# Optimization experiments

Hardware: AMD Instinct MI355X
Metric: run time of the kernel (lower is better)

Reference implementation:

```python
import jax, jax.numpy as jnp
import numpy as np

N_NODES = 50000
N_EDGES = 800000
ENT_DIM = 128
REL_DIM = 128
NUM_REL = 200  # relation table has 2*NUM_REL rows (forward + inverse)


def setup_inputs() -> dict:
    key = jax.random.key(0)
    ks = jax.random.split(key, 16)
    inp = {
        'src': jax.random.randint(ks[0], (N_EDGES,), 0, N_NODES),
        'dst': jax.random.randint(ks[1], (N_EDGES,), 0, N_NODES),
        'etypes': jax.random.randint(ks[2], (N_EDGES,), 0, 2 * NUM_REL),
        'ent_emb': jax.random.normal(ks[3], (N_NODES, ENT_DIM), jnp.float32),
        'rel_emb': jax.random.normal(ks[4], (2 * NUM_REL, REL_DIM), jnp.float32),
        'W_O_w': jax.random.normal(ks[5], (ENT_DIM, REL_DIM + ENT_DIM), jnp.float32) * 0.05,
        'W_O_b': jax.random.normal(ks[6], (ENT_DIM,), jnp.float32) * 0.05,
        'W_I_w': jax.random.normal(ks[7], (ENT_DIM, REL_DIM + ENT_DIM), jnp.float32) * 0.05,
        'W_I_b': jax.random.normal(ks[8], (ENT_DIM,), jnp.float32) * 0.05,
        'W_S_w': jax.random.normal(ks[9], (ENT_DIM, ENT_DIM), jnp.float32) * 0.05,
        'W_S_b': jax.random.normal(ks[10], (ENT_DIM,), jnp.float32) * 0.05,
        'W_R_w': jax.random.normal(ks[11], (REL_DIM, REL_DIM), jnp.float32) * 0.05,
        'W_R_b': jax.random.normal(ks[12], (REL_DIM,), jnp.float32) * 0.05,
    }
    return inp


def reference(src, dst, etypes, ent_emb, rel_emb,
              W_O_w, W_O_b, W_I_w, W_I_b, W_S_w, W_S_b, W_R_w, W_R_b):
    # msg_func: per-edge gather of relation emb and source node emb, concat,
    # then route through W_O (type < num_rel) or W_I (type >= num_rel).
    comp_h = jnp.concatenate([rel_emb[etypes], ent_emb[src]], axis=-1)  # [E, rel+ent]
    msg_o = comp_h @ W_O_w.T + W_O_b  # [E, ent]
    msg_i = comp_h @ W_I_w.T + W_I_b
    non_inv = (etypes < NUM_REL)[:, None]
    msg = jnp.where(non_inv, msg_o, msg_i)
    # fn.mean('msg','h_agg'): scatter-mean into destination nodes (0 if no in-edges)
    agg_sum = jax.ops.segment_sum(msg, dst, num_segments=N_NODES)
    deg = jax.ops.segment_sum(jnp.ones((msg.shape[0],), msg.dtype), dst,
                              num_segments=N_NODES)
    h_agg = agg_sum / jnp.maximum(deg, 1.0)[:, None]
    # apply_node_func (act is None -> identity)
    ent_new = ent_emb @ W_S_w.T + W_S_b + h_agg
    # edge_update
    rel_new = rel_emb @ W_R_w.T + W_R_b
    return ent_new, rel_new
```

## Files before the change

kernel.cpp:

```cpp
#include <hip/hip_runtime.h>
#include <hip/hip_bf16.h>

#define N_NODES 50000
#define N_EDGES 800000
#define DIM 128
#define NUM_REL 200
#define NREL2 (2 * NUM_REL)
#define NROWG (N_NODES / 16)
#define NBLK_G ((NROWG + 3) / 4)
#define FILL_NB 2048
#define NCHUNK_E (N_EDGES / 256)
#define NODES_PER_XCD (N_NODES / 8)
#define CAP 64
#define ZROW (2 * N_NODES)
#define ZREL NREL2
#define ZPAY (ZROW | (ZREL << 17))

typedef __bf16 bf16x8 __attribute__((ext_vector_type(8)));
typedef float f32x4 __attribute__((ext_vector_type(4)));

__global__ void __launch_bounds__(256)
prep_rel_kernel(const float* __restrict__ rel_emb,
                const float* __restrict__ W_O_w, const float* __restrict__ W_O_b,
                const float* __restrict__ W_I_w, const float* __restrict__ W_I_b,
                const float* __restrict__ W_R_w, const float* __restrict__ W_R_b,
                const float* __restrict__ W_S_w,
                __bf16* __restrict__ WTh, __bf16* __restrict__ WTl,
                int* __restrict__ counts, __bf16* __restrict__ EEb,
                __bf16* __restrict__ Rb, float* __restrict__ rel_new) {
    const int bid = blockIdx.x;
    if (bid < NREL2 / 2) {
        __shared__ float row[2][DIM];
        const int h = threadIdx.x >> 7;
        const int j = threadIdx.x & 127;
        const int t = bid * 2 + h;
        row[h][j] = rel_emb[t * DIM + j];
        __syncthreads();

        const bool fwd = (t < NUM_REL);
        const float* __restrict__ wSel = (fwd ? W_O_w : W_I_w) + j * (2 * DIM);
        const float* __restrict__ wR = W_R_w + j * DIM;
        float aSel = 0.f, aR = 0.f;
#pragma unroll 8
        for (int k = 0; k < DIM; ++k) {
            const float e = row[h][k];
            aSel += e * wSel[k];
            aR += e * wR[k];
        }
        Rb[t * DIM + j] = (__bf16)(aSel + (fwd ? W_O_b[j] : W_I_b[j]));
        rel_new[t * DIM + j] = aR + W_R_b[j];
    } else {
        const int idx = (bid - NREL2 / 2) * 256 + threadIdx.x;
        if (idx < 384 * DIM) {
            const int j = idx >> 7;
            const int k = idx & 127;
            float v;
            if (j < 128) v = W_O_w[j * (2 * DIM) + DIM + k];
            else if (j < 256) v = W_I_w[(j - 128) * (2 * DIM) + DIM + k];
            else v = W_S_w[(j - 256) * DIM + k];
            const __bf16 h = (__bf16)v;
            WTh[idx] = h;
            WTl[idx] = (__bf16)(v - (float)h);
        }
        if (idx < N_NODES) counts[idx] = 0;
        if (idx < DIM) {
            EEb[(size_t)ZROW * DIM + idx] = (__bf16)0.f;
            Rb[(size_t)ZREL * DIM + idx] = (__bf16)0.f;
        }
    }
}

#define REP4(F) F(0) F(1) F(2) F(3)

__global__ void __launch_bounds__(256, 1)
gemm_fill_kernel(const float* __restrict__ ent,
                 const __bf16* __restrict__ WTh, const __bf16* __restrict__ WTl,
                 const float* __restrict__ W_S_b,
                 __bf16* __restrict__ EEb, float* __restrict__ ent_S,
                 const int* __restrict__ src, const int* __restrict__ dst,
                 const int* __restrict__ et, int* __restrict__ counts,
                 int* __restrict__ sp) {
    __shared__ __bf16 LBh[16 * 64 * 8];
    __shared__ __bf16 LBl[16 * 64 * 8];

    if (blockIdx.x >= NBLK_G) {
        const int fb = blockIdx.x - NBLK_G;
        const int r = blockIdx.x & 7;
#pragma unroll 1
        for (int c = fb >> 3; c < NCHUNK_E; c += FILL_NB / 8) {
            const int e = c * 256 + threadIdx.x;
            const int d = dst[e];
            if ((unsigned)(d - r * NODES_PER_XCD) < (unsigned)NODES_PER_XCD) {
                const int t = et[e];
                const int row = src[e] + ((t < NUM_REL) ? 0 : N_NODES);
                const int pos = atomicAdd(&counts[d], 1);
                if (pos < CAP) sp[(d << 6) + pos] = row | (t << 17);
            }
        }
        return;
    }

    const int tid = threadIdx.x;
    const int wv = tid >> 6;
    const int rg = blockIdx.x * 4 + wv;
    const bool valid = (rg < NROWG);
    const int rgc = valid ? rg : (NROWG - 1);
    const int l = tid & 63;
    const int r16 = l & 15;
    const int kg = l >> 4;

    const float* __restrict__ aptr = ent + (size_t)(rgc * 16 + r16) * DIM + kg * 8;
#define ADECL(ks)                                                              \
    bf16x8 ah##ks, al##ks;                                                     \
    {                                                                          \
        const float4 v0 = *(const float4*)(aptr + (ks) * 32);                  \
        const float4 v1 = *(const float4*)(aptr + (ks) * 32 + 4);              \
        const float xs[8] = {v0.x, v0.y, v0.z, v0.w, v1.x, v1.y, v1.z, v1.w};  \
        _Pragma("unroll") for (int i = 0; i < 8; ++i) {                        \
            const __bf16 h = (__bf16)xs[i];                                    \
            ah##ks[i] = h;                                                     \
            al##ks[i] = (__bf16)(xs[i] - (float)h);                            \
        }                                                                      \
    }
    REP4(ADECL)
#undef ADECL

    const int orow = rgc * 16 + kg * 4;

#pragma unroll 1
    for (int cb = 0; cb < 6; ++cb) {
        __syncthreads();
#pragma unroll
        for (int i = 0; i < 4; ++i) {
            const int sks = i * 4 + wv;
            const int s = sks >> 2;
            const int ks = sks & 3;
            const size_t soff =
                (size_t)(cb * 64 + s * 16 + r16) * DIM + ks * 32 + kg * 8;
            const int g = i * 256 + tid;
            *(bf16x8*)(&LBh[g * 8]) = *(const bf16x8*)(WTh + soff);
            *(bf16x8*)(&LBl[g * 8]) = *(const bf16x8*)(WTl + soff);
        }
        __syncthreads();

        f32x4 p0 = {0.f, 0.f, 0.f, 0.f}, q0 = {0.f, 0.f, 0.f, 0.f};
        f32x4 p1 = {0.f, 0.f, 0.f, 0.f}, q1 = {0.f, 0.f, 0.f, 0.f};
        f32x4 p2 = {0.f, 0.f, 0.f, 0.f}, q2 = {0.f, 0.f, 0.f, 0.f};
        f32x4 p3 = {0.f, 0.f, 0.f, 0.f}, q3 = {0.f, 0.f, 0.f, 0.f};

#define KS(ks)                                                                 \
    {                                                                          \
        const bf16x8 bh0 = *(const bf16x8*)(&LBh[((0 * 4 + (ks)) * 64 + l) * 8]); \
        const bf16x8 bh1 = *(const bf16x8*)(&LBh[((1 * 4 + (ks)) * 64 + l) * 8]); \
        const bf16x8 bh2 = *(const bf16x8*)(&LBh[((2 * 4 + (ks)) * 64 + l) * 8]); \
        const bf16x8 bh3 = *(const bf16x8*)(&LBh[((3 * 4 + (ks)) * 64 + l) * 8]); \
        const bf16x8 bl0 = *(const bf16x8*)(&LBl[((0 * 4 + (ks)) * 64 + l) * 8]); \
        const bf16x8 bl1 = *(const bf16x8*)(&LBl[((1 * 4 + (ks)) * 64 + l) * 8]); \
        const bf16x8 bl2 = *(const bf16x8*)(&LBl[((2 * 4 + (ks)) * 64 + l) * 8]); \
        const bf16x8 bl3 = *(const bf16x8*)(&LBl[((3 * 4 + (ks)) * 64 + l) * 8]); \
        p0 = __builtin_amdgcn_mfma_f32_16x16x32_bf16(ah##ks, bh0, p0, 0, 0, 0); \
        p1 = __builtin_amdgcn_mfma_f32_16x16x32_bf16(ah##ks, bh1, p1, 0, 0, 0); \
        p2 = __builtin_amdgcn_mfma_f32_16x16x32_bf16(ah##ks, bh2, p2, 0, 0, 0); \
        p3 = __builtin_amdgcn_mfma_f32_16x16x32_bf16(ah##ks, bh3, p3, 0, 0, 0); \
        q0 = __builtin_amdgcn_mfma_f32_16x16x32_bf16(al##ks, bh0, q0, 0, 0, 0); \
        q1 = __builtin_amdgcn_mfma_f32_16x16x32_bf16(al##ks, bh1, q1, 0, 0, 0); \
        q2 = __builtin_amdgcn_mfma_f32_16x16x32_bf16(al##ks, bh2, q2, 0, 0, 0); \
        q3 = __builtin_amdgcn_mfma_f32_16x16x32_bf16(al##ks, bh3, q3, 0, 0, 0); \
        q0 = __builtin_amdgcn_mfma_f32_16x16x32_bf16(ah##ks, bl0, q0, 0, 0, 0); \
        q1 = __builtin_amdgcn_mfma_f32_16x16x32_bf16(ah##ks, bl1, q1, 0, 0, 0); \
        q2 = __builtin_amdgcn_mfma_f32_16x16x32_bf16(ah##ks, bl2, q2, 0, 0, 0); \
        q3 = __builtin_amdgcn_mfma_f32_16x16x32_bf16(ah##ks, bl3, q3, 0, 0, 0); \
    }
        REP4(KS)
#undef KS

        if (valid) {
            const int colb = (cb & 1) * 64;
            if (cb < 4) {
                __bf16* __restrict__ obb =
                    EEb + ((cb < 2) ? 0 : (size_t)N_NODES * DIM);
#define ST(s, P, Q)                                                            \
                {                                                              \
                    const int col = colb + (s) * 16 + r16;                     \
                    const f32x4 a = P + Q;                                     \
                    obb[(size_t)(orow + 0) * DIM + col] = (__bf16)a[0];        \
                    obb[(size_t)(orow + 1) * DIM + col] = (__bf16)a[1];        \
                    obb[(size_t)(orow + 2) * DIM + col] = (__bf16)a[2];        \
                    obb[(size_t)(orow + 3) * DIM + col] = (__bf16)a[3];        \
                }
                ST(0, p0, q0) ST(1, p1, q1) ST(2, p2, q2) ST(3, p3, q3)
#undef ST
            } else {
#define ST(s, P, Q)                                                            \
                {                                                              \
                    const int col = colb + (s) * 16 + r16;                     \
                    const float bs = W_S_b[col];                               \
                    const f32x4 a = P + Q;                                     \
                    ent_S[(size_t)(orow + 0) * DIM + col] = a[0] + bs;         \
                    ent_S[(size_t)(orow + 1) * DIM + col] = a[1] + bs;         \
                    ent_S[(size_t)(orow + 2) * DIM + col] = a[2] + bs;         \
                    ent_S[(size_t)(orow + 3) * DIM + col] = a[3] + bs;         \
                }
                ST(0, p0, q0) ST(1, p1, q1) ST(2, p2, q2) ST(3, p3, q3)
#undef ST
            }
        }
    }
}

__global__ void __launch_bounds__(256)
gather_kernel(const int* __restrict__ counts, const int* __restrict__ sp,
              const __bf16* __restrict__ EEb, const __bf16* __restrict__ Rb,
              const float* __restrict__ ent_S, float* __restrict__ out_ent) {
    const int node = blockIdx.x * 4 + (threadIdx.x >> 6);
    if (node >= N_NODES) return;
    const int l = threadIdx.x & 63;
    const int q = l >> 4;
    const int m = l & 15;

    const int cntT = counts[node];
    const int cnt = min(cntT, CAP);

    float a0 = 0.f, a1 = 0.f, a2 = 0.f, a3 = 0.f;
    float a4 = 0.f, a5 = 0.f, a6 = 0.f, a7 = 0.f;
    const char* __restrict__ Eb = (const char*)EEb + 16 * m;
    const char* __restrict__ Rp = (const char*)Rb + 16 * m;

    const int myp = (l < cnt) ? sp[(node << 6) + l] : ZPAY;
#pragma unroll 2
    for (int i = 0; i < cnt; i += 4) {
        const int p = __shfl(myp, i + q);
        const unsigned eoff = (unsigned)(p & 0x1FFFF) << 8;
        const unsigned roff = ((unsigned)p >> 17) << 8;
        const uint4 ev = *(const uint4*)(Eb + eoff);
        const uint4 rv = *(const uint4*)(Rp + roff);
        a0 += __uint_as_float(ev.x << 16) + __uint_as_float(rv.x << 16);
        a1 += __uint_as_float(ev.x & 0xffff0000u) +
              __uint_as_float(rv.x & 0xffff0000u);
        a2 += __uint_as_float(ev.y << 16) + __uint_as_float(rv.y << 16);
        a3 += __uint_as_float(ev.y & 0xffff0000u) +
              __uint_as_float(rv.y & 0xffff0000u);
        a4 += __uint_as_float(ev.z << 16) + __uint_as_float(rv.z << 16);
        a5 += __uint_as_float(ev.z & 0xffff0000u) +
              __uint_as_float(rv.z & 0xffff0000u);
        a6 += __uint_as_float(ev.w << 16) + __uint_as_float(rv.w << 16);
        a7 += __uint_as_float(ev.w & 0xffff0000u) +
              __uint_as_float(rv.w & 0xffff0000u);
    }

#define RED(A) A += __shfl_xor(A, 16); A += __shfl_xor(A, 32);
    RED(a0) RED(a1) RED(a2) RED(a3) RED(a4) RED(a5) RED(a6) RED(a7)
#undef RED

    if (l < 16) {
        const float inv = 1.0f / fmaxf((float)cntT, 1.0f);
        const float* sp_ = ent_S + (size_t)node * DIM + 8 * m;
        const float4 s0 = *(const float4*)(sp_);
        const float4 s1 = *(const float4*)(sp_ + 4);
        float4 o0, o1;
        o0.x = s0.x + a0 * inv;
        o0.y = s0.y + a1 * inv;
        o0.z = s0.z + a2 * inv;
        o0.w = s0.w + a3 * inv;
        o1.x = s1.x + a4 * inv;
        o1.y = s1.y + a5 * inv;
        o1.z = s1.z + a6 * inv;
        o1.w = s1.w + a7 * inv;
        float* op = out_ent + (size_t)node * DIM + 8 * m;
        *(float4*)(op) = o0;
        *(float4*)(op + 4) = o1;
    }
}

extern "C" void kernel_launch(void* const* d_in, const int* in_sizes, int n_in,
                              void* d_out, int out_size, void* d_ws, size_t ws_size,
                              hipStream_t stream) {
    const int* src = (const int*)d_in[0];
    const int* dst = (const int*)d_in[1];
    const int* et = (const int*)d_in[2];
    const float* ent_emb = (const float*)d_in[3];
    const float* rel_emb = (const float*)d_in[4];
    const float* W_O_w = (const float*)d_in[5];
    const float* W_O_b = (const float*)d_in[6];
    const float* W_I_w = (const float*)d_in[7];
    const float* W_I_b = (const float*)d_in[8];
    const float* W_S_w = (const float*)d_in[9];
    const float* W_S_b = (const float*)d_in[10];
    const float* W_R_w = (const float*)d_in[11];
    const float* W_R_b = (const float*)d_in[12];

    float* out_ent = (float*)d_out;
    float* out_rel = out_ent + (size_t)N_NODES * DIM;

    float* wsf = (float*)d_ws;
    float* ent_S = wsf;
    wsf += (size_t)N_NODES * DIM;
    __bf16* EEb = (__bf16*)wsf;
    wsf += ((size_t)(2 * N_NODES + 1) * DIM + 1) / 2;
    __bf16* Rb = (__bf16*)wsf;
    wsf += (size_t)(NREL2 + 1) * DIM / 2;
    __bf16* WTh = (__bf16*)wsf;
    wsf += 384 * DIM / 2;
    __bf16* WTl = (__bf16*)wsf;
    wsf += 384 * DIM / 2;
    int* counts = (int*)wsf;
    int* sp = counts + N_NODES;

    prep_rel_kernel<<<NREL2 / 2 + 196, 256, 0, stream>>>(
        rel_emb, W_O_w, W_O_b, W_I_w, W_I_b, W_R_w, W_R_b, W_S_w,
        WTh, WTl, counts, EEb, Rb, out_rel);

    gemm_fill_kernel<<<NBLK_G + FILL_NB, 256, 0, stream>>>(
        ent_emb, WTh, WTl, W_S_b, EEb, ent_S, src, dst, et, counts, sp);

    gather_kernel<<<(N_NODES + 3) / 4, 256, 0, stream>>>(counts, sp, EEb, Rb,
                                                         ent_S, out_ent);
}
```

Baseline: 121.1 us.

## Halve weight LDS staging into two phases and reduce fill block count

The weight tile staged in LDS per column block is split into two half-size phases, each staging two of the four output sub-tiles before computing them. This halves LDS usage, which could let more GEMM blocks reside per CU, at the cost of an extra pair of barriers per column block. The edge-fill block count is also halved from 2048 to 1024, changing how the fill work is split across blocks.

```diff
diff --git a/kernel.cpp b/kernel.cpp
--- a/kernel.cpp
+++ b/kernel.cpp
@@ -8,7 +8,7 @@
 #define NREL2 (2 * NUM_REL)
 #define NROWG (N_NODES / 16)
 #define NBLK_G ((NROWG + 3) / 4)
-#define FILL_NB 2048
+#define FILL_NB 1024
 #define NCHUNK_E (N_EDGES / 256)
 #define NODES_PER_XCD (N_NODES / 8)
 #define CAP 64
@@ -80,8 +80,8 @@
                  const int* __restrict__ src, const int* __restrict__ dst,
                  const int* __restrict__ et, int* __restrict__ counts,
                  int* __restrict__ sp) {
-    __shared__ __bf16 LBh[16 * 64 * 8];
-    __shared__ __bf16 LBl[16 * 64 * 8];
+    __shared__ __bf16 LBh[8 * 64 * 8];
+    __shared__ __bf16 LBl[8 * 64 * 8];
 
     if (blockIdx.x >= NBLK_G) {
         const int fb = blockIdx.x - NBLK_G;
@@ -129,50 +129,53 @@
 
 #pragma unroll 1
     for (int cb = 0; cb < 6; ++cb) {
-        __syncthreads();
-#pragma unroll
-        for (int i = 0; i < 4; ++i) {
-            const int sks = i * 4 + wv;
-            const int s = sks >> 2;
-            const int ks = sks & 3;
-            const size_t soff =
-                (size_t)(cb * 64 + s * 16 + r16) * DIM + ks * 32 + kg * 8;
-            const int g = i * 256 + tid;
-            *(bf16x8*)(&LBh[g * 8]) = *(const bf16x8*)(WTh + soff);
-            *(bf16x8*)(&LBl[g * 8]) = *(const bf16x8*)(WTl + soff);
-        }
-        __syncthreads();
-
         f32x4 p0 = {0.f, 0.f, 0.f, 0.f}, q0 = {0.f, 0.f, 0.f, 0.f};
         f32x4 p1 = {0.f, 0.f, 0.f, 0.f}, q1 = {0.f, 0.f, 0.f, 0.f};
         f32x4 p2 = {0.f, 0.f, 0.f, 0.f}, q2 = {0.f, 0.f, 0.f, 0.f};
         f32x4 p3 = {0.f, 0.f, 0.f, 0.f}, q3 = {0.f, 0.f, 0.f, 0.f};
 
-#define KS(ks)                                                                 \
+#define STAGE_PH(ph)                                                           \
+        __syncthreads();                                                       \
+        _Pragma("unroll") for (int i = 0; i < 2; ++i) {                        \
+            const int g = i * 256 + tid;                           \
+            const int sks2 = g >> 6;                                 \
+            const int ls = g & 63;                                             \
+            const int ksS = sks2 & 3;                                          \
+            const int sS = (ph) * 2 + (sks2 >> 2);                             \
+            const size_t soff = (size_t)(cb * 64 + sS * 16 + (ls & 15)) * DIM  \
+                                + ksS * 32 + (ls >> 4) * 8;                    \
+            *(bf16x8*)(&LBh[g * 8]) = *(const bf16x8*)(WTh + soff);            \
+            *(bf16x8*)(&LBl[g * 8]) = *(const bf16x8*)(WTl + soff);            \
+        }                                                                      \
+        __syncthreads();
+
+#define KS2(ks, Pa, Qa, Pb, Qb)                                                \
     {                                                                          \
-        const bf16x8 bh0 = *(const bf16x8*)(&LBh[((0 * 4 + (ks)) * 64 + l) * 8]); \
-        const bf16x8 bh1 = *(const bf16x8*)(&LBh[((1 * 4 + (ks)) * 64 + l) * 8]); \
-        const bf16x8 bh2 = *(const bf16x8*)(&LBh[((2 * 4 + (ks)) * 64 + l) * 8]); \
-        const bf16x8 bh3 = *(const bf16x8*)(&LBh[((3 * 4 + (ks)) * 64 + l) * 8]); \
-        const bf16x8 bl0 = *(const bf16x8*)(&LBl[((0 * 4 + (ks)) * 64 + l) * 8]); \
-        const bf16x8 bl1 = *(const bf16x8*)(&LBl[((1 * 4 + (ks)) * 64 + l) * 8]); \
-        const bf16x8 bl2 = *(const bf16x8*)(&LBl[((2 * 4 + (ks)) * 64 + l) * 8]); \
-        const bf16x8 bl3 = *(const bf16x8*)(&LBl[((3 * 4 + (ks)) * 64 + l) * 8]); \
-        p0 = __builtin_amdgcn_mfma_f32_16x16x32_bf16(ah##ks, bh0, p0, 0, 0, 0); \
-        p1 = __builtin_amdgcn_mfma_f32_16x16x32_bf16(ah##ks, bh1, p1, 0, 0, 0); \
-        p2 = __builtin_amdgcn_mfma_f32_16x16x32_bf16(ah##ks, bh2, p2, 0, 0, 0); \
-        p3 = __builtin_amdgcn_mfma_f32_16x16x32_bf16(ah##ks, bh3, p3, 0, 0, 0); \
-        q0 = __builtin_amdgcn_mfma_f32_16x16x32_bf16(al##ks, bh0, q0, 0, 0, 0); \
-        q1 = __builtin_amdgcn_mfma_f32_16x16x32_bf16(al##ks, bh1, q1, 0, 0, 0); \
-        q2 = __builtin_amdgcn_mfma_f32_16x16x32_bf16(al##ks, bh2, q2, 0, 0, 0); \
-        q3 = __builtin_amdgcn_mfma_f32_16x16x32_bf16(al##ks, bh3, q3, 0, 0, 0); \
-        q0 = __builtin_amdgcn_mfma_f32_16x16x32_bf16(ah##ks, bl0, q0, 0, 0, 0); \
-        q1 = __builtin_amdgcn_mfma_f32_16x16x32_bf16(ah##ks, bl1, q1, 0, 0, 0); \
-        q2 = __builtin_amdgcn_mfma_f32_16x16x32_bf16(ah##ks, bl2, q2, 0, 0, 0); \
-        q3 = __builtin_amdgcn_mfma_f32_16x16x32_bf16(ah##ks, bl3, q3, 0, 0, 0); \
-    }
-        REP4(KS)
-#undef KS
+        const bf16x8 bha = *(const bf16x8*)(&LBh[((0 * 4 + (ks)) * 64 + l) * 8]); \
+        const bf16x8 bhb = *(const bf16x8*)(&LBh[((1 * 4 + (ks)) * 64 + l) * 8]); \
+        const bf16x8 bla = *(const bf16x8*)(&LBl[((0 * 4 + (ks)) * 64 + l) * 8]); \
+        const bf16x8 blb = *(const bf16x8*)(&LBl[((1 * 4 + (ks)) * 64 + l) * 8]); \
+        Pa = __builtin_amdgcn_mfma_f32_16x16x32_bf16(ah##ks, bha, Pa, 0, 0, 0); \
+        Pb = __builtin_amdgcn_mfma_f32_16x16x32_bf16(ah##ks, bhb, Pb, 0, 0, 0); \
+        Qa = __builtin_amdgcn_mfma_f32_16x16x32_bf16(al##ks, bha, Qa, 0, 0, 0); \
+        Qb = __builtin_amdgcn_mfma_f32_16x16x32_bf16(al##ks, bhb, Qb, 0, 0, 0); \
+        Qa = __builtin_amdgcn_mfma_f32_16x16x32_bf16(ah##ks, bla, Qa, 0, 0, 0); \
+        Qb = __builtin_amdgcn_mfma_f32_16x16x32_bf16(ah##ks, blb, Qb, 0, 0, 0); \
+    }
+
+        STAGE_PH(0)
+        KS2(0, p0, q0, p1, q1)
+        KS2(1, p0, q0, p1, q1)
+        KS2(2, p0, q0, p1, q1)
+        KS2(3, p0, q0, p1, q1)
+
+        STAGE_PH(1)
+        KS2(0, p2, q2, p3, q3)
+        KS2(1, p2, q2, p3, q3)
+        KS2(2, p2, q2, p3, q3)
+        KS2(3, p2, q2, p3, q3)
+#undef KS2
+#undef STAGE_PH
 
         if (valid) {
             const int colb = (cb & 1) * 64;
```

Measured after the change: 130.9 us. +8.1%, slower.
